# Kernel tuning notes

Measured on AMD Instinct MI355X. Metric: run time of the kernel, lower is better.

The kernel has to match this reference:

```python
import jax, jax.numpy as jnp
import numpy as np

N, D_IN, D_OUT, B = 200000, 256, 256, 256

def setup_inputs() -> dict:
    key = jax.random.key(0)
    k1, k2, k3, k4, k5 = jax.random.split(key, 5)
    lim = float(np.sqrt(6.0 / (D_IN + D_OUT)))  # xavier_init scale=1
    return {
        "nodes": jax.random.normal(k1, (N, D_IN), dtype=jnp.float32),
        "owner_masks": jax.random.randint(k2, (B, N), 0, 2, dtype=jnp.int32),
        "Wt": jax.random.uniform(k3, (D_OUT, D_IN), jnp.float32, -lim, lim),
        "bt": jax.random.normal(k4, (D_OUT,), dtype=jnp.float32),
        "Wg": jax.random.uniform(k5, (D_OUT, D_IN), jnp.float32, -lim, lim),
        "bg": jnp.ones((D_OUT,), dtype=jnp.float32),  # gate bias init fill_(1)
    }

def reference(nodes, owner_masks, Wt, bt, Wg, bg):
    # gates = sigmoid(Linear(nodes)); data = Linear(nodes)  -> [N, D_OUT]
    gates = jax.nn.sigmoid(nodes @ Wg.T + bg)
    data = nodes @ Wt.T + bt
    # owner-mask matmul == masked scatter-sum over nodes -> [B, D_OUT]
    fmask = owner_masks.astype(jnp.float32)
    res = jnp.einsum('bn,nd->bd', fmask, data * gates)
    return res  # dropout is identity in eval mode
```

## Files before the change

### kernel.cpp

```cpp
#include <hip/hip_runtime.h>
#include <stdint.h>

#define NND 200000

typedef unsigned short u16;
typedef __attribute__((ext_vector_type(4))) float f4;
typedef __attribute__((ext_vector_type(4))) int   i4;
typedef __attribute__((ext_vector_type(2))) unsigned int u2;
typedef __attribute__((ext_vector_type(8))) short s8;
typedef __attribute__((ext_vector_type(4))) float acc4;

__device__ __forceinline__ short f2bf(float f) {
    union { float f; uint32_t u; } v; v.f = f;
    uint32_t r = v.u + 0x7FFFu + ((v.u >> 16) & 1u);
    return (short)(r >> 16);
}
__device__ __forceinline__ uint32_t pack2bf(float a, float b) {
    uint32_t ua = __float_as_uint(a), ub = __float_as_uint(b);
    ua = ua + 0x7FFFu + ((ua >> 16) & 1u);
    ub = ub + 0x7FFFu + ((ub >> 16) & 1u);
    return (ua >> 16) | (ub & 0xFFFF0000u);
}
__device__ __forceinline__ void gld16(const void* g, void* l) {
    __builtin_amdgcn_global_load_lds(
        (const __attribute__((address_space(1))) void*)g,
        (__attribute__((address_space(3))) void*)l, 16, 0, 0);
}
__device__ __forceinline__ void bar_lgkm() {
    asm volatile("s_waitcnt lgkmcnt(0)" ::: "memory");
    __builtin_amdgcn_s_barrier();
    asm volatile("" ::: "memory");
}

__global__ __launch_bounds__(256) void k_prep(const float* __restrict__ Wt,
                                              const float* __restrict__ Wg,
                                              u16* __restrict__ wtb,
                                              u16* __restrict__ wgb) {
    int i = blockIdx.x * 256 + threadIdx.x;
    wtb[i] = (u16)f2bf(Wt[i]);
    wgb[i] = (u16)f2bf(Wg[i]);
}

__global__ __launch_bounds__(1024, 4) void k_h(const float* __restrict__ nodes,
                                               const u16* __restrict__ wtb,
                                               const u16* __restrict__ wgb,
                                               const float* __restrict__ btp,
                                               const float* __restrict__ bgp,
                                               u16* __restrict__ h_t) {
    __shared__ __align__(16) char smem[69632];
    char* A0 = smem;
    char* A1 = smem + 16384;
    char* H0 = smem + 32768;
    char* H1 = smem + 51200;

    const int tid  = threadIdx.x;
    const int lane = tid & 63, wave = tid >> 6;
    const int quad = lane >> 4, l16 = lane & 15;
    const int dgl  = wave * 16 + l16;

    s8 wT[8], wG[8];
    {
        const u16* wtp = wtb + dgl * 256 + quad * 8;
        const u16* wgp = wgb + dgl * 256 + quad * 8;
#pragma unroll
        for (int ks = 0; ks < 8; ++ks) {
            wT[ks] = *(const s8*)(wtp + ks * 32);
            wG[ks] = *(const s8*)(wgp + ks * 32);
        }
    }
    const float btv = btp[dgl], bgv = bgp[dgl];

    const int bid = blockIdx.x;
    const int NC  = (bid < 250) ? 13 : 12;
    const int c0  = (bid < 250) ? bid * 13 : 3250 + (bid - 250) * 12;

    const int arow = tid >> 5, akq = tid & 31;
    const int awbyte = akq * 512 + (((arow & 24) | ((arow ^ akq) & 7)) << 4);
    const int sd = tid >> 2, sc = tid & 3;

    f4 ar0, ar1;
    {
        const f4* p = (const f4*)(nodes + (size_t)(c0 * 32 + arow) * 256 + akq * 8);
        ar0 = p[0]; ar1 = p[1];
        i4 aw;
        aw.x = (int)pack2bf(ar0.x, ar0.y); aw.y = (int)pack2bf(ar0.z, ar0.w);
        aw.z = (int)pack2bf(ar1.x, ar1.y); aw.w = (int)pack2bf(ar1.z, ar1.w);
        *(i4*)(A0 + awbyte) = aw;
        const f4* q = (const f4*)(nodes + (size_t)((c0 + 1) * 32 + arow) * 256 + akq * 8);
        ar0 = q[0]; ar1 = q[1];
    }
    bar_lgkm();

    char *Ard = A0, *Awr = A1, *Hwr = H0, *Hrd = H1;

    for (int c = 0; c < NC; ++c) {
        acc4 at0 = (acc4)0.0f, at1 = (acc4)0.0f, ag0 = (acc4)0.0f, ag1 = (acc4)0.0f;
#pragma unroll
        for (int ks = 0; ks < 8; ++ks) {
            const int kq = ks * 4 + quad;
            const int ab = kq * 512 + (((l16 & 8) | ((l16 ^ kq) & 7)) << 4);
            s8 af0 = *(const s8*)(Ard + ab);
            s8 af1 = *(const s8*)(Ard + ab + 256);
            at0 = __builtin_amdgcn_mfma_f32_16x16x32_bf16(af0, wT[ks], at0, 0, 0, 0);
            ag0 = __builtin_amdgcn_mfma_f32_16x16x32_bf16(af0, wG[ks], ag0, 0, 0, 0);
            at1 = __builtin_amdgcn_mfma_f32_16x16x32_bf16(af1, wT[ks], at1, 0, 0, 0);
            ag1 = __builtin_amdgcn_mfma_f32_16x16x32_bf16(af1, wG[ks], ag1, 0, 0, 0);
        }
        if (c < NC - 1) {
            i4 aw;
            aw.x = (int)pack2bf(ar0.x, ar0.y); aw.y = (int)pack2bf(ar0.z, ar0.w);
            aw.z = (int)pack2bf(ar1.x, ar1.y); aw.w = (int)pack2bf(ar1.z, ar1.w);
            *(i4*)(Awr + awbyte) = aw;
        }
        if (c < NC - 2) {
            const f4* p = (const f4*)(nodes + (size_t)((c0 + c + 2) * 32 + arow) * 256 + akq * 8);
            ar0 = p[0]; ar1 = p[1];
        }
#pragma unroll
        for (int rt = 0; rt < 2; ++rt) {
            const acc4 t = rt ? at1 : at0;
            const acc4 g = rt ? ag1 : ag0;
            float h0 = (t[0] + btv) / (1.0f + __expf(-(g[0] + bgv)));
            float h1 = (t[1] + btv) / (1.0f + __expf(-(g[1] + bgv)));
            float h2 = (t[2] + btv) / (1.0f + __expf(-(g[2] + bgv)));
            float h3 = (t[3] + btv) / (1.0f + __expf(-(g[3] + bgv)));
            u2 p; p.x = pack2bf(h0, h1); p.y = pack2bf(h2, h3);
            *(u2*)(Hwr + dgl * 72 + rt * 32 + quad * 8) = p;
        }
        if (c > 0) {
            f4 v = *(const f4*)(Hrd + sd * 72 + sc * 16);
            *(f4*)(h_t + (size_t)sd * NND + (size_t)(c0 + c - 1) * 32 + sc * 8) = v;
        }
        bar_lgkm();
        char* tp = Ard; Ard = Awr; Awr = tp;
        tp = Hwr; Hwr = Hrd; Hrd = tp;
    }
    {
        f4 v = *(const f4*)(Hrd + sd * 72 + sc * 16);
        *(f4*)(h_t + (size_t)sd * NND + (size_t)(c0 + NC - 1) * 32 + sc * 8) = v;
    }
}

__global__ __launch_bounds__(1024, 4) void k_res(const int* __restrict__ masks,
                                                 const u16* __restrict__ h_t,
                                                 float* __restrict__ outp) {
    __shared__ __align__(16) char smem[131072];
    char* Ms0 = smem;
    char* Hs0 = smem + 65536;

    const int tid  = threadIdx.x;
    const int lane = tid & 63, wave = tid >> 6;
    const int quad = lane >> 4, l16 = lane & 15;
    const int bh = wave & 3, dq = wave >> 2;

    const int bid = blockIdx.x;
    const int R   = 12 + (bid < 53 ? 1 : 0);
    const int it0 = bid * 12 + min(bid, 53);

    acc4 acc[4][4];
#pragma unroll
    for (int rt = 0; rt < 4; ++rt)
#pragma unroll
        for (int dt = 0; dt < 4; ++dt) acc[rt][dt] = (acc4)0.0f;

    const int mr = tid >> 2, seg = tid & 3;
    const size_t mrow = (size_t)mr * NND;

    i4 mp[4];
    {
        const int nb = it0 * 64;
        const i4* p = (const i4*)(masks + mrow + nb + seg * 16);
        mp[0] = p[0]; mp[1] = p[1]; mp[2] = p[2]; mp[3] = p[3];
#pragma unroll
        for (int i = 0; i < 2; ++i) {
            int g = i * 1024 + tid;
            int dr = g >> 3, c = g & 7;
            gld16(h_t + (size_t)dr * NND + nb + ((c ^ (dr & 7)) << 3), Hs0 + g * 16);
        }
    }

    int cur = 0;
    for (int it = 0; it < R; ++it) {
        const int nb = (it0 + it) * 64;
        {
            uint32_t w0 = (((uint32_t)(-mp[0].x)) & 0x3F80u) | ((((uint32_t)(-mp[0].y)) & 0x3F80u) << 16);
            uint32_t w1 = (((uint32_t)(-mp[0].z)) & 0x3F80u) | ((((uint32_t)(-mp[0].w)) & 0x3F80u) << 16);
            uint32_t w2 = (((uint32_t)(-mp[1].x)) & 0x3F80u) | ((((uint32_t)(-mp[1].y)) & 0x3F80u) << 16);
            uint32_t w3 = (((uint32_t)(-mp[1].z)) & 0x3F80u) | ((((uint32_t)(-mp[1].w)) & 0x3F80u) << 16);
            uint32_t w4 = (((uint32_t)(-mp[2].x)) & 0x3F80u) | ((((uint32_t)(-mp[2].y)) & 0x3F80u) << 16);
            uint32_t w5 = (((uint32_t)(-mp[2].z)) & 0x3F80u) | ((((uint32_t)(-mp[2].w)) & 0x3F80u) << 16);
            uint32_t w6 = (((uint32_t)(-mp[3].x)) & 0x3F80u) | ((((uint32_t)(-mp[3].y)) & 0x3F80u) << 16);
            uint32_t w7 = (((uint32_t)(-mp[3].z)) & 0x3F80u) | ((((uint32_t)(-mp[3].w)) & 0x3F80u) << 16);
            i4 a, b;
            a.x = (int)w0; a.y = (int)w1; a.z = (int)w2; a.w = (int)w3;
            b.x = (int)w4; b.y = (int)w5; b.z = (int)w6; b.w = (int)w7;
            char* base = Ms0 + cur * 32768 + mr * 128;
            const int g0 = seg * 2;
            *(i4*)(base + (((g0    ) ^ (mr & 7)) << 4)) = a;
            *(i4*)(base + (((g0 + 1) ^ (mr & 7)) << 4)) = b;
        }
        if (it + 1 < R) {
            const i4* p = (const i4*)(masks + mrow + (nb + 64) + seg * 16);
            mp[0] = p[0]; mp[1] = p[1]; mp[2] = p[2]; mp[3] = p[3];
        }
        bar_lgkm();
        if (it + 1 < R) {
#pragma unroll
            for (int i = 0; i < 2; ++i) {
                int g = i * 1024 + tid;
                int dr = g >> 3, c = g & 7;
                gld16(h_t + (size_t)dr * NND + (nb + 64) + ((c ^ (dr & 7)) << 3),
                      Hs0 + (cur ^ 1) * 32768 + g * 16);
            }
            asm volatile("s_waitcnt vmcnt(6)" ::: "memory");
        } else {
            asm volatile("s_waitcnt vmcnt(0)" ::: "memory");
        }
        __builtin_amdgcn_sched_barrier(0);
        const char* Mr = Ms0 + cur * 32768;
        const char* Hr = Hs0 + cur * 32768;
#pragma unroll
        for (int ks = 0; ks < 2; ++ks) {
            const int q = (ks << 2) | quad;
            s8 af[4];
#pragma unroll
            for (int rt = 0; rt < 4; ++rt) {
                int r = bh * 64 + rt * 16 + l16;
                af[rt] = *(const s8*)(Mr + r * 128 + ((q ^ (r & 7)) << 4));
            }
#pragma unroll
            for (int dt = 0; dt < 4; ++dt) {
                int dl = dq * 64 + dt * 16 + l16;
                s8 bf_ = *(const s8*)(Hr + dl * 128 + ((q ^ (dl & 7)) << 4));
#pragma unroll
                for (int rt = 0; rt < 4; ++rt)
                    acc[rt][dt] = __builtin_amdgcn_mfma_f32_16x16x32_bf16(af[rt], bf_, acc[rt][dt], 0, 0, 0);
            }
        }
        cur ^= 1;
    }
#pragma unroll
    for (int rt = 0; rt < 4; ++rt)
#pragma unroll
        for (int dt = 0; dt < 4; ++dt) {
            int b = bh * 64 + rt * 16 + quad * 4;
            int d = dq * 64 + dt * 16 + l16;
#pragma unroll
            for (int r = 0; r < 4; ++r)
                atomicAdd(outp + (size_t)(b + r) * 256 + d, acc[rt][dt][r]);
        }
}

extern "C" void kernel_launch(void* const* d_in, const int* in_sizes, int n_in,
                              void* d_out, int out_size, void* d_ws, size_t ws_size,
                              hipStream_t stream) {
    const float* nodes = (const float*)d_in[0];
    const int*   masks = (const int*)d_in[1];
    const float* Wt    = (const float*)d_in[2];
    const float* bt    = (const float*)d_in[3];
    const float* Wg    = (const float*)d_in[4];
    const float* bg    = (const float*)d_in[5];
    float* outp = (float*)d_out;

    u16* h_t = (u16*)d_ws;
    u16* wtb = (u16*)((char*)d_ws + (size_t)102400000);
    u16* wgb = wtb + 65536;

    hipMemsetAsync(d_out, 0, (size_t)out_size * sizeof(float), stream);
    k_prep<<<dim3(256), dim3(256), 0, stream>>>(Wt, Wg, wtb, wgb);
    k_h<<<dim3(500), dim3(1024), 0, stream>>>(nodes, wtb, wgb, bt, bg, h_t);
    k_res<<<dim3(256), dim3(1024), 0, stream>>>(masks, h_t, outp);
}
```

Baseline: 513.4 us.

## Deepen prefetch pipelines, resize k_h grid, replace atomics with partial-sum reduction kernel

```diff
diff --git a/kernel.cpp b/kernel.cpp
--- a/kernel.cpp
+++ b/kernel.cpp
@@ -71,23 +71,30 @@
     const float btv = btp[dgl], bgv = bgp[dgl];
 
     const int bid = blockIdx.x;
-    const int NC  = (bid < 250) ? 13 : 12;
-    const int c0  = (bid < 250) ? bid * 13 : 3250 + (bid - 250) * 12;
+    const int NC  = (bid < 106) ? 25 : 24;
+    const int c0  = (bid < 106) ? bid * 25 : 2650 + (bid - 106) * 24;
 
     const int arow = tid >> 5, akq = tid & 31;
     const int awbyte = akq * 512 + (((arow & 24) | ((arow ^ akq) & 7)) << 4);
     const int sd = tid >> 2, sc = tid & 3;
-
-    f4 ar0, ar1;
-    {
-        const f4* p = (const f4*)(nodes + (size_t)(c0 * 32 + arow) * 256 + akq * 8);
-        ar0 = p[0]; ar1 = p[1];
+    const float* abase = nodes + (size_t)arow * 256 + akq * 8;
+
+    f4 s1a, s1b, s2a, s2b, s3a, s3b;
+    {
+        const f4* p = (const f4*)(abase + (size_t)(c0) * 32 * 256);
+        f4 t0 = p[0], t1 = p[1];
         i4 aw;
-        aw.x = (int)pack2bf(ar0.x, ar0.y); aw.y = (int)pack2bf(ar0.z, ar0.w);
-        aw.z = (int)pack2bf(ar1.x, ar1.y); aw.w = (int)pack2bf(ar1.z, ar1.w);
+        aw.x = (int)pack2bf(t0.x, t0.y); aw.y = (int)pack2bf(t0.z, t0.w);
+        aw.z = (int)pack2bf(t1.x, t1.y); aw.w = (int)pack2bf(t1.z, t1.w);
         *(i4*)(A0 + awbyte) = aw;
-        const f4* q = (const f4*)(nodes + (size_t)((c0 + 1) * 32 + arow) * 256 + akq * 8);
-        ar0 = q[0]; ar1 = q[1];
+    }
+    {
+        const f4* p1 = (const f4*)(abase + (size_t)(c0 + 1) * 32 * 256);
+        s1a = p1[0]; s1b = p1[1];
+        const f4* p2 = (const f4*)(abase + (size_t)(c0 + 2) * 32 * 256);
+        s2a = p2[0]; s2b = p2[1];
+        const f4* p3 = (const f4*)(abase + (size_t)(c0 + 3) * 32 * 256);
+        s3a = p3[0]; s3b = p3[1];
     }
     bar_lgkm();
 
@@ -106,15 +113,17 @@
             at1 = __builtin_amdgcn_mfma_f32_16x16x32_bf16(af1, wT[ks], at1, 0, 0, 0);
             ag1 = __builtin_amdgcn_mfma_f32_16x16x32_bf16(af1, wG[ks], ag1, 0, 0, 0);
         }
-        if (c < NC - 1) {
+        if (c + 1 < NC) {
             i4 aw;
-            aw.x = (int)pack2bf(ar0.x, ar0.y); aw.y = (int)pack2bf(ar0.z, ar0.w);
-            aw.z = (int)pack2bf(ar1.x, ar1.y); aw.w = (int)pack2bf(ar1.z, ar1.w);
+            aw.x = (int)pack2bf(s1a.x, s1a.y); aw.y = (int)pack2bf(s1a.z, s1a.w);
+            aw.z = (int)pack2bf(s1b.x, s1b.y); aw.w = (int)pack2bf(s1b.z, s1b.w);
             *(i4*)(Awr + awbyte) = aw;
         }
-        if (c < NC - 2) {
-            const f4* p = (const f4*)(nodes + (size_t)((c0 + c + 2) * 32 + arow) * 256 + akq * 8);
-            ar0 = p[0]; ar1 = p[1];
+        s1a = s2a; s1b = s2b;
+        s2a = s3a; s2b = s3b;
+        if (c + 4 < NC) {
+            const f4* p = (const f4*)(abase + (size_t)(c0 + c + 4) * 32 * 256);
+            s3a = p[0]; s3b = p[1];
         }
 #pragma unroll
         for (int rt = 0; rt < 2; ++rt) {
@@ -143,7 +152,7 @@
 
 __global__ __launch_bounds__(1024, 4) void k_res(const int* __restrict__ masks,
                                                  const u16* __restrict__ h_t,
-                                                 float* __restrict__ outp) {
+                                                 float* __restrict__ partials) {
     __shared__ __align__(16) char smem[131072];
     char* Ms0 = smem;
     char* Hs0 = smem + 65536;
@@ -165,12 +174,16 @@
 
     const int mr = tid >> 2, seg = tid & 3;
     const size_t mrow = (size_t)mr * NND;
-
-    i4 mp[4];
+    const int g0 = seg * 2;
+    char* msrow = Ms0 + mr * 128;
+
+    i4 m1[4], m2[4];
     {
         const int nb = it0 * 64;
         const i4* p = (const i4*)(masks + mrow + nb + seg * 16);
-        mp[0] = p[0]; mp[1] = p[1]; mp[2] = p[2]; mp[3] = p[3];
+        m1[0] = p[0]; m1[1] = p[1]; m1[2] = p[2]; m1[3] = p[3];
+        const i4* q = (const i4*)(masks + mrow + nb + 64 + seg * 16);
+        m2[0] = q[0]; m2[1] = q[1]; m2[2] = q[2]; m2[3] = q[3];
 #pragma unroll
         for (int i = 0; i < 2; ++i) {
             int g = i * 1024 + tid;
@@ -183,25 +196,25 @@
     for (int it = 0; it < R; ++it) {
         const int nb = (it0 + it) * 64;
         {
-            uint32_t w0 = (((uint32_t)(-mp[0].x)) & 0x3F80u) | ((((uint32_t)(-mp[0].y)) & 0x3F80u) << 16);
-            uint32_t w1 = (((uint32_t)(-mp[0].z)) & 0x3F80u) | ((((uint32_t)(-mp[0].w)) & 0x3F80u) << 16);
-            uint32_t w2 = (((uint32_t)(-mp[1].x)) & 0x3F80u) | ((((uint32_t)(-mp[1].y)) & 0x3F80u) << 16);
-            uint32_t w3 = (((uint32_t)(-mp[1].z)) & 0x3F80u) | ((((uint32_t)(-mp[1].w)) & 0x3F80u) << 16);
-            uint32_t w4 = (((uint32_t)(-mp[2].x)) & 0x3F80u) | ((((uint32_t)(-mp[2].y)) & 0x3F80u) << 16);
-            uint32_t w5 = (((uint32_t)(-mp[2].z)) & 0x3F80u) | ((((uint32_t)(-mp[2].w)) & 0x3F80u) << 16);
-            uint32_t w6 = (((uint32_t)(-mp[3].x)) & 0x3F80u) | ((((uint32_t)(-mp[3].y)) & 0x3F80u) << 16);
-            uint32_t w7 = (((uint32_t)(-mp[3].z)) & 0x3F80u) | ((((uint32_t)(-mp[3].w)) & 0x3F80u) << 16);
+            uint32_t w0 = (((uint32_t)(-m1[0].x)) & 0x3F80u) | ((((uint32_t)(-m1[0].y)) & 0x3F80u) << 16);
+            uint32_t w1 = (((uint32_t)(-m1[0].z)) & 0x3F80u) | ((((uint32_t)(-m1[0].w)) & 0x3F80u) << 16);
+            uint32_t w2 = (((uint32_t)(-m1[1].x)) & 0x3F80u) | ((((uint32_t)(-m1[1].y)) & 0x3F80u) << 16);
+            uint32_t w3 = (((uint32_t)(-m1[1].z)) & 0x3F80u) | ((((uint32_t)(-m1[1].w)) & 0x3F80u) << 16);
+            uint32_t w4 = (((uint32_t)(-m1[2].x)) & 0x3F80u) | ((((uint32_t)(-m1[2].y)) & 0x3F80u) << 16);
+            uint32_t w5 = (((uint32_t)(-m1[2].z)) & 0x3F80u) | ((((uint32_t)(-m1[2].w)) & 0x3F80u) << 16);
+            uint32_t w6 = (((uint32_t)(-m1[3].x)) & 0x3F80u) | ((((uint32_t)(-m1[3].y)) & 0x3F80u) << 16);
+            uint32_t w7 = (((uint32_t)(-m1[3].z)) & 0x3F80u) | ((((uint32_t)(-m1[3].w)) & 0x3F80u) << 16);
             i4 a, b;
             a.x = (int)w0; a.y = (int)w1; a.z = (int)w2; a.w = (int)w3;
             b.x = (int)w4; b.y = (int)w5; b.z = (int)w6; b.w = (int)w7;
-            char* base = Ms0 + cur * 32768 + mr * 128;
-            const int g0 = seg * 2;
+            char* base = msrow + cur * 32768;
             *(i4*)(base + (((g0    ) ^ (mr & 7)) << 4)) = a;
             *(i4*)(base + (((g0 + 1) ^ (mr & 7)) << 4)) = b;
         }
-        if (it + 1 < R) {
-            const i4* p = (const i4*)(masks + mrow + (nb + 64) + seg * 16);
-            mp[0] = p[0]; mp[1] = p[1]; mp[2] = p[2]; mp[3] = p[3];
+        m1[0] = m2[0]; m1[1] = m2[1]; m1[2] = m2[2]; m1[3] = m2[3];
+        if (it + 2 < R) {
+            const i4* p = (const i4*)(masks + mrow + (nb + 128) + seg * 16);
+            m2[0] = p[0]; m2[1] = p[1]; m2[2] = p[2]; m2[3] = p[3];
         }
         bar_lgkm();
         if (it + 1 < R) {
@@ -239,6 +252,7 @@
         }
         cur ^= 1;
     }
+    float* pb = partials + (size_t)bid * 65536;
 #pragma unroll
     for (int rt = 0; rt < 4; ++rt)
 #pragma unroll
@@ -247,8 +261,28 @@
             int d = dq * 64 + dt * 16 + l16;
 #pragma unroll
             for (int r = 0; r < 4; ++r)
-                atomicAdd(outp + (size_t)(b + r) * 256 + d, acc[rt][dt][r]);
-        }
+                pb[(size_t)(b + r) * 256 + d] = acc[rt][dt][r];
+        }
+}
+
+__global__ __launch_bounds__(1024) void k_red(const float* __restrict__ partials,
+                                              float* __restrict__ outp) {
+    __shared__ float red[4][256];
+    const int b = blockIdx.x;
+    const int d = threadIdx.x & 255, ks = threadIdx.x >> 8;
+    const float* p = partials + (size_t)(ks * 64) * 65536 + b * 256 + d;
+    float s0 = 0.f, s1 = 0.f, s2 = 0.f, s3 = 0.f;
+#pragma unroll 4
+    for (int j = 0; j < 64; j += 4) {
+        s0 += p[(size_t)(j + 0) * 65536];
+        s1 += p[(size_t)(j + 1) * 65536];
+        s2 += p[(size_t)(j + 2) * 65536];
+        s3 += p[(size_t)(j + 3) * 65536];
+    }
+    red[ks][d] = (s0 + s1) + (s2 + s3);
+    __syncthreads();
+    if (ks == 0)
+        outp[b * 256 + d] = (red[0][d] + red[1][d]) + (red[2][d] + red[3][d]);
 }
 
 extern "C" void kernel_launch(void* const* d_in, const int* in_sizes, int n_in,
@@ -262,12 +296,13 @@
     const float* bg    = (const float*)d_in[5];
     float* outp = (float*)d_out;
 
-    u16* h_t = (u16*)d_ws;
-    u16* wtb = (u16*)((char*)d_ws + (size_t)102400000);
-    u16* wgb = wtb + 65536;
-
-    hipMemsetAsync(d_out, 0, (size_t)out_size * sizeof(float), stream);
+    u16*   h_t  = (u16*)d_ws;
+    u16*   wtb  = (u16*)((char*)d_ws + (size_t)102400000);
+    u16*   wgb  = wtb + 65536;
+    float* part = (float*)((char*)d_ws + (size_t)102531072);
+
     k_prep<<<dim3(256), dim3(256), 0, stream>>>(Wt, Wg, wtb, wgb);
-    k_h<<<dim3(500), dim3(1024), 0, stream>>>(nodes, wtb, wgb, bt, bg, h_t);
-    k_res<<<dim3(256), dim3(1024), 0, stream>>>(masks, h_t, outp);
-}
+    k_h<<<dim3(256), dim3(1024), 0, stream>>>(nodes, wtb, wgb, bt, bg, h_t);
+    k_res<<<dim3(256), dim3(1024), 0, stream>>>(masks, h_t, part);
+    k_red<<<dim3(256), dim3(1024), 0, stream>>>(part, outp);
+}
```

Result: slower. 559.8 us (+9.0%).

## Fuse gated linear and mask matmul into one kernel, reduce partials separately

Applied to the files above, without the earlier changes.

```diff
diff --git a/kernel.cpp b/kernel.cpp
--- a/kernel.cpp
+++ b/kernel.cpp
@@ -20,11 +20,6 @@
     ua = ua + 0x7FFFu + ((ua >> 16) & 1u);
     ub = ub + 0x7FFFu + ((ub >> 16) & 1u);
     return (ua >> 16) | (ub & 0xFFFF0000u);
-}
-__device__ __forceinline__ void gld16(const void* g, void* l) {
-    __builtin_amdgcn_global_load_lds(
-        (const __attribute__((address_space(1))) void*)g,
-        (__attribute__((address_space(3))) void*)l, 16, 0, 0);
 }
 __device__ __forceinline__ void bar_lgkm() {
     asm volatile("s_waitcnt lgkmcnt(0)" ::: "memory");
@@ -41,22 +36,23 @@
     wgb[i] = (u16)f2bf(Wg[i]);
 }
 
-__global__ __launch_bounds__(1024, 4) void k_h(const float* __restrict__ nodes,
-                                               const u16* __restrict__ wtb,
-                                               const u16* __restrict__ wgb,
-                                               const float* __restrict__ btp,
-                                               const float* __restrict__ bgp,
-                                               u16* __restrict__ h_t) {
-    __shared__ __align__(16) char smem[69632];
-    char* A0 = smem;
-    char* A1 = smem + 16384;
-    char* H0 = smem + 32768;
-    char* H1 = smem + 51200;
+__global__ __launch_bounds__(1024, 2) void k_main(const float* __restrict__ nodes,
+                                                  const int* __restrict__ masks,
+                                                  const u16* __restrict__ wtb,
+                                                  const u16* __restrict__ wgb,
+                                                  const float* __restrict__ btp,
+                                                  const float* __restrict__ bgp,
+                                                  float* __restrict__ partials) {
+    __shared__ __align__(16) char smem[98304];
+    char* As = smem;
+    char* Ms = smem + 32768;
+    char* Hs = smem + 65536;
 
     const int tid  = threadIdx.x;
     const int lane = tid & 63, wave = tid >> 6;
     const int quad = lane >> 4, l16 = lane & 15;
     const int dgl  = wave * 16 + l16;
+    const int bh = wave & 3, dq = wave >> 2;
 
     s8 wT[8], wG[8];
     {
@@ -71,117 +67,45 @@
     const float btv = btp[dgl], bgv = bgp[dgl];
 
     const int bid = blockIdx.x;
-    const int NC  = (bid < 250) ? 13 : 12;
-    const int c0  = (bid < 250) ? bid * 13 : 3250 + (bid - 250) * 12;
-
-    const int arow = tid >> 5, akq = tid & 31;
-    const int awbyte = akq * 512 + (((arow & 24) | ((arow ^ akq) & 7)) << 4);
-    const int sd = tid >> 2, sc = tid & 3;
-
-    f4 ar0, ar1;
-    {
-        const f4* p = (const f4*)(nodes + (size_t)(c0 * 32 + arow) * 256 + akq * 8);
-        ar0 = p[0]; ar1 = p[1];
-        i4 aw;
-        aw.x = (int)pack2bf(ar0.x, ar0.y); aw.y = (int)pack2bf(ar0.z, ar0.w);
-        aw.z = (int)pack2bf(ar1.x, ar1.y); aw.w = (int)pack2bf(ar1.z, ar1.w);
-        *(i4*)(A0 + awbyte) = aw;
-        const f4* q = (const f4*)(nodes + (size_t)((c0 + 1) * 32 + arow) * 256 + akq * 8);
-        ar0 = q[0]; ar1 = q[1];
-    }
-    bar_lgkm();
-
-    char *Ard = A0, *Awr = A1, *Hwr = H0, *Hrd = H1;
-
-    for (int c = 0; c < NC; ++c) {
-        acc4 at0 = (acc4)0.0f, at1 = (acc4)0.0f, ag0 = (acc4)0.0f, ag1 = (acc4)0.0f;
-#pragma unroll
-        for (int ks = 0; ks < 8; ++ks) {
-            const int kq = ks * 4 + quad;
-            const int ab = kq * 512 + (((l16 & 8) | ((l16 ^ kq) & 7)) << 4);
-            s8 af0 = *(const s8*)(Ard + ab);
-            s8 af1 = *(const s8*)(Ard + ab + 256);
-            at0 = __builtin_amdgcn_mfma_f32_16x16x32_bf16(af0, wT[ks], at0, 0, 0, 0);
-            ag0 = __builtin_amdgcn_mfma_f32_16x16x32_bf16(af0, wG[ks], ag0, 0, 0, 0);
-            at1 = __builtin_amdgcn_mfma_f32_16x16x32_bf16(af1, wT[ks], at1, 0, 0, 0);
-            ag1 = __builtin_amdgcn_mfma_f32_16x16x32_bf16(af1, wG[ks], ag1, 0, 0, 0);
-        }
-        if (c < NC - 1) {
-            i4 aw;
-            aw.x = (int)pack2bf(ar0.x, ar0.y); aw.y = (int)pack2bf(ar0.z, ar0.w);
-            aw.z = (int)pack2bf(ar1.x, ar1.y); aw.w = (int)pack2bf(ar1.z, ar1.w);
-            *(i4*)(Awr + awbyte) = aw;
-        }
-        if (c < NC - 2) {
-            const f4* p = (const f4*)(nodes + (size_t)((c0 + c + 2) * 32 + arow) * 256 + akq * 8);
-            ar0 = p[0]; ar1 = p[1];
-        }
-#pragma unroll
-        for (int rt = 0; rt < 2; ++rt) {
-            const acc4 t = rt ? at1 : at0;
-            const acc4 g = rt ? ag1 : ag0;
-            float h0 = (t[0] + btv) / (1.0f + __expf(-(g[0] + bgv)));
-            float h1 = (t[1] + btv) / (1.0f + __expf(-(g[1] + bgv)));
-            float h2 = (t[2] + btv) / (1.0f + __expf(-(g[2] + bgv)));
-            float h3 = (t[3] + btv) / (1.0f + __expf(-(g[3] + bgv)));
-            u2 p; p.x = pack2bf(h0, h1); p.y = pack2bf(h2, h3);
-            *(u2*)(Hwr + dgl * 72 + rt * 32 + quad * 8) = p;
-        }
-        if (c > 0) {
-            f4 v = *(const f4*)(Hrd + sd * 72 + sc * 16);
-            *(f4*)(h_t + (size_t)sd * NND + (size_t)(c0 + c - 1) * 32 + sc * 8) = v;
-        }
-        bar_lgkm();
-        char* tp = Ard; Ard = Awr; Awr = tp;
-        tp = Hwr; Hwr = Hrd; Hrd = tp;
-    }
-    {
-        f4 v = *(const f4*)(Hrd + sd * 72 + sc * 16);
-        *(f4*)(h_t + (size_t)sd * NND + (size_t)(c0 + NC - 1) * 32 + sc * 8) = v;
-    }
-}
-
-__global__ __launch_bounds__(1024, 4) void k_res(const int* __restrict__ masks,
-                                                 const u16* __restrict__ h_t,
-                                                 float* __restrict__ outp) {
-    __shared__ __align__(16) char smem[131072];
-    char* Ms0 = smem;
-    char* Hs0 = smem + 65536;
-
-    const int tid  = threadIdx.x;
-    const int lane = tid & 63, wave = tid >> 6;
-    const int quad = lane >> 4, l16 = lane & 15;
-    const int bh = wave & 3, dq = wave >> 2;
-
-    const int bid = blockIdx.x;
-    const int R   = 12 + (bid < 53 ? 1 : 0);
+    const int NC  = 12 + (bid < 53 ? 1 : 0);
     const int it0 = bid * 12 + min(bid, 53);
 
-    acc4 acc[4][4];
-#pragma unroll
-    for (int rt = 0; rt < 4; ++rt)
-#pragma unroll
-        for (int dt = 0; dt < 4; ++dt) acc[rt][dt] = (acc4)0.0f;
-
+    const int arow = tid >> 4, aseg = tid & 15;
+    const float* abase = nodes + (size_t)arow * 256 + aseg * 16;
     const int mr = tid >> 2, seg = tid & 3;
     const size_t mrow = (size_t)mr * NND;
-
+    const int g0 = seg * 2;
+    char* msrow = Ms + mr * 128;
+
+    acc4 acc[4][4];
+#pragma unroll
+    for (int rt = 0; rt < 4; ++rt)
+#pragma unroll
+        for (int dt = 0; dt < 4; ++dt) acc[rt][dt] = (acc4)0.0f;
+
+    f4 a0, a1, a2, a3;
     i4 mp[4];
     {
         const int nb = it0 * 64;
-        const i4* p = (const i4*)(masks + mrow + nb + seg * 16);
-        mp[0] = p[0]; mp[1] = p[1]; mp[2] = p[2]; mp[3] = p[3];
-#pragma unroll
-        for (int i = 0; i < 2; ++i) {
-            int g = i * 1024 + tid;
-            int dr = g >> 3, c = g & 7;
-            gld16(h_t + (size_t)dr * NND + nb + ((c ^ (dr & 7)) << 3), Hs0 + g * 16);
-        }
-    }
-
-    int cur = 0;
-    for (int it = 0; it < R; ++it) {
-        const int nb = (it0 + it) * 64;
+        const f4* p = (const f4*)(abase + (size_t)nb * 256);
+        a0 = p[0]; a1 = p[1]; a2 = p[2]; a3 = p[3];
+        const i4* q = (const i4*)(masks + mrow + nb + seg * 16);
+        mp[0] = q[0]; mp[1] = q[1]; mp[2] = q[2]; mp[3] = q[3];
+        i4 w0, w1;
+        w0.x = (int)pack2bf(a0.x, a0.y); w0.y = (int)pack2bf(a0.z, a0.w);
+        w0.z = (int)pack2bf(a1.x, a1.y); w0.w = (int)pack2bf(a1.z, a1.w);
+        w1.x = (int)pack2bf(a2.x, a2.y); w1.y = (int)pack2bf(a2.z, a2.w);
+        w1.z = (int)pack2bf(a3.x, a3.y); w1.w = (int)pack2bf(a3.z, a3.w);
+        const int ga = aseg * 2, gb = ga + 1;
+        *(i4*)(As + ga * 1024 + (((arow & 56) | ((arow ^ ga) & 7)) << 4)) = w0;
+        *(i4*)(As + gb * 1024 + (((arow & 56) | ((arow ^ gb) & 7)) << 4)) = w1;
+        const f4* p1 = (const f4*)(abase + (size_t)(nb + 64) * 256);
+        a0 = p1[0]; a1 = p1[1]; a2 = p1[2]; a3 = p1[3];
+    }
+    bar_lgkm();
+
+    for (int c = 0; c < NC; ++c) {
+        const int nb = (it0 + c) * 64;
         {
             uint32_t w0 = (((uint32_t)(-mp[0].x)) & 0x3F80u) | ((((uint32_t)(-mp[0].y)) & 0x3F80u) << 16);
             uint32_t w1 = (((uint32_t)(-mp[0].z)) & 0x3F80u) | ((((uint32_t)(-mp[0].w)) & 0x3F80u) << 16);
@@ -191,64 +115,106 @@
             uint32_t w5 = (((uint32_t)(-mp[2].z)) & 0x3F80u) | ((((uint32_t)(-mp[2].w)) & 0x3F80u) << 16);
             uint32_t w6 = (((uint32_t)(-mp[3].x)) & 0x3F80u) | ((((uint32_t)(-mp[3].y)) & 0x3F80u) << 16);
             uint32_t w7 = (((uint32_t)(-mp[3].z)) & 0x3F80u) | ((((uint32_t)(-mp[3].w)) & 0x3F80u) << 16);
-            i4 a, b;
-            a.x = (int)w0; a.y = (int)w1; a.z = (int)w2; a.w = (int)w3;
-            b.x = (int)w4; b.y = (int)w5; b.z = (int)w6; b.w = (int)w7;
-            char* base = Ms0 + cur * 32768 + mr * 128;
-            const int g0 = seg * 2;
-            *(i4*)(base + (((g0    ) ^ (mr & 7)) << 4)) = a;
-            *(i4*)(base + (((g0 + 1) ^ (mr & 7)) << 4)) = b;
-        }
-        if (it + 1 < R) {
-            const i4* p = (const i4*)(masks + mrow + (nb + 64) + seg * 16);
-            mp[0] = p[0]; mp[1] = p[1]; mp[2] = p[2]; mp[3] = p[3];
+            i4 ma, mb;
+            ma.x = (int)w0; ma.y = (int)w1; ma.z = (int)w2; ma.w = (int)w3;
+            mb.x = (int)w4; mb.y = (int)w5; mb.z = (int)w6; mb.w = (int)w7;
+            *(i4*)(msrow + (((g0    ) ^ (mr & 7)) << 4)) = ma;
+            *(i4*)(msrow + (((g0 + 1) ^ (mr & 7)) << 4)) = mb;
+        }
+        if (c + 1 < NC) {
+            const i4* q = (const i4*)(masks + mrow + (nb + 64) + seg * 16);
+            mp[0] = q[0]; mp[1] = q[1]; mp[2] = q[2]; mp[3] = q[3];
+        }
+        acc4 at_[4], ag_[4];
+#pragma unroll
+        for (int rt = 0; rt < 4; ++rt) { at_[rt] = (acc4)0.0f; ag_[rt] = (acc4)0.0f; }
+#pragma unroll
+        for (int ks = 0; ks < 8; ++ks) {
+            const int kq = ks * 4 + quad;
+#pragma unroll
+            for (int rt = 0; rt < 4; ++rt) {
+                const int row = rt * 16 + l16;
+                s8 af = *(const s8*)(As + kq * 1024 + (((row & 56) | ((row ^ kq) & 7)) << 4));
+                at_[rt] = __builtin_amdgcn_mfma_f32_16x16x32_bf16(af, wT[ks], at_[rt], 0, 0, 0);
+                ag_[rt] = __builtin_amdgcn_mfma_f32_16x16x32_bf16(af, wG[ks], ag_[rt], 0, 0, 0);
+            }
+        }
+#pragma unroll
+        for (int rt = 0; rt < 4; ++rt) {
+            float h0 = (at_[rt][0] + btv) / (1.0f + __expf(-(ag_[rt][0] + bgv)));
+            float h1 = (at_[rt][1] + btv) / (1.0f + __expf(-(ag_[rt][1] + bgv)));
+            float h2 = (at_[rt][2] + btv) / (1.0f + __expf(-(ag_[rt][2] + bgv)));
+            float h3 = (at_[rt][3] + btv) / (1.0f + __expf(-(ag_[rt][3] + bgv)));
+            u2 pk; pk.x = pack2bf(h0, h1); pk.y = pack2bf(h2, h3);
+            const int g = rt * 2 + (quad >> 1);
+            *(u2*)(Hs + dgl * 128 + ((g ^ (dgl & 7)) << 4) + (quad & 1) * 8) = pk;
         }
         bar_lgkm();
-        if (it + 1 < R) {
-#pragma unroll
-            for (int i = 0; i < 2; ++i) {
-                int g = i * 1024 + tid;
-                int dr = g >> 3, c = g & 7;
-                gld16(h_t + (size_t)dr * NND + (nb + 64) + ((c ^ (dr & 7)) << 3),
-                      Hs0 + (cur ^ 1) * 32768 + g * 16);
-            }
-            asm volatile("s_waitcnt vmcnt(6)" ::: "memory");
-        } else {
-            asm volatile("s_waitcnt vmcnt(0)" ::: "memory");
-        }
-        __builtin_amdgcn_sched_barrier(0);
-        const char* Mr = Ms0 + cur * 32768;
-        const char* Hr = Hs0 + cur * 32768;
 #pragma unroll
         for (int ks = 0; ks < 2; ++ks) {
             const int q = (ks << 2) | quad;
             s8 af[4];
 #pragma unroll
             for (int rt = 0; rt < 4; ++rt) {
-                int r = bh * 64 + rt * 16 + l16;
-                af[rt] = *(const s8*)(Mr + r * 128 + ((q ^ (r & 7)) << 4));
+                const int r = bh * 64 + rt * 16 + l16;
+                af[rt] = *(const s8*)(Ms + r * 128 + ((q ^ (r & 7)) << 4));
             }
 #pragma unroll
             for (int dt = 0; dt < 4; ++dt) {
-                int dl = dq * 64 + dt * 16 + l16;
-                s8 bf_ = *(const s8*)(Hr + dl * 128 + ((q ^ (dl & 7)) << 4));
+                const int dl = dq * 64 + dt * 16 + l16;
+                s8 bf_ = *(const s8*)(Hs + dl * 128 + ((q ^ (dl & 7)) << 4));
 #pragma unroll
                 for (int rt = 0; rt < 4; ++rt)
                     acc[rt][dt] = __builtin_amdgcn_mfma_f32_16x16x32_bf16(af[rt], bf_, acc[rt][dt], 0, 0, 0);
             }
         }
-        cur ^= 1;
-    }
+        if (c + 1 < NC) {
+            i4 w0, w1;
+            w0.x = (int)pack2bf(a0.x, a0.y); w0.y = (int)pack2bf(a0.z, a0.w);
+            w0.z = (int)pack2bf(a1.x, a1.y); w0.w = (int)pack2bf(a1.z, a1.w);
+            w1.x = (int)pack2bf(a2.x, a2.y); w1.y = (int)pack2bf(a2.z, a2.w);
+            w1.z = (int)pack2bf(a3.x, a3.y); w1.w = (int)pack2bf(a3.z, a3.w);
+            const int ga = aseg * 2, gb = ga + 1;
+            *(i4*)(As + ga * 1024 + (((arow & 56) | ((arow ^ ga) & 7)) << 4)) = w0;
+            *(i4*)(As + gb * 1024 + (((arow & 56) | ((arow ^ gb) & 7)) << 4)) = w1;
+            if (c + 2 < NC) {
+                const f4* p = (const f4*)(abase + (size_t)(nb + 128) * 256);
+                a0 = p[0]; a1 = p[1]; a2 = p[2]; a3 = p[3];
+            }
+        }
+        bar_lgkm();
+    }
+    float* pb = partials + (size_t)bid * 65536;
 #pragma unroll
     for (int rt = 0; rt < 4; ++rt)
 #pragma unroll
         for (int dt = 0; dt < 4; ++dt) {
-            int b = bh * 64 + rt * 16 + quad * 4;
-            int d = dq * 64 + dt * 16 + l16;
+            const int b = bh * 64 + rt * 16 + quad * 4;
+            const int d = dq * 64 + dt * 16 + l16;
 #pragma unroll
             for (int r = 0; r < 4; ++r)
-                atomicAdd(outp + (size_t)(b + r) * 256 + d, acc[rt][dt][r]);
-        }
+                pb[(size_t)(b + r) * 256 + d] = acc[rt][dt][r];
+        }
+}
+
+__global__ __launch_bounds__(1024) void k_red(const float* __restrict__ partials,
+                                              float* __restrict__ outp) {
+    __shared__ float red[4][256];
+    const int b = blockIdx.x;
+    const int d = threadIdx.x & 255, ks = threadIdx.x >> 8;
+    const float* p = partials + (size_t)(ks * 64) * 65536 + b * 256 + d;
+    float s0 = 0.f, s1 = 0.f, s2 = 0.f, s3 = 0.f;
+#pragma unroll 4
+    for (int j = 0; j < 64; j += 4) {
+        s0 += p[(size_t)(j + 0) * 65536];
+        s1 += p[(size_t)(j + 1) * 65536];
+        s2 += p[(size_t)(j + 2) * 65536];
+        s3 += p[(size_t)(j + 3) * 65536];
+    }
+    red[ks][d] = (s0 + s1) + (s2 + s3);
+    __syncthreads();
+    if (ks == 0)
+        outp[b * 256 + d] = (red[0][d] + red[1][d]) + (red[2][d] + red[3][d]);
 }
 
 extern "C" void kernel_launch(void* const* d_in, const int* in_sizes, int n_in,
@@ -262,12 +228,11 @@
     const float* bg    = (const float*)d_in[5];
     float* outp = (float*)d_out;
 
-    u16* h_t = (u16*)d_ws;
-    u16* wtb = (u16*)((char*)d_ws + (size_t)102400000);
-    u16* wgb = wtb + 65536;
-
-    hipMemsetAsync(d_out, 0, (size_t)out_size * sizeof(float), stream);
+    u16*   wtb  = (u16*)d_ws;
+    u16*   wgb  = wtb + 65536;
+    float* part = (float*)((char*)d_ws + 262144);
+
     k_prep<<<dim3(256), dim3(256), 0, stream>>>(Wt, Wg, wtb, wgb);
-    k_h<<<dim3(500), dim3(1024), 0, stream>>>(nodes, wtb, wgb, bt, bg, h_t);
-    k_res<<<dim3(256), dim3(1024), 0, stream>>>(masks, h_t, outp);
-}
+    k_main<<<dim3(256), dim3(1024), 0, stream>>>(nodes, masks, wtb, wgb, bt, bg, part);
+    k_red<<<dim3(256), dim3(1024), 0, stream>>>(part, outp);
+}
```

New measurement: 746.7 us. 45.4% more time.
